# Optimization experiments

Measured on AMD Instinct MI355X. Metric: run time of the kernel, lower is better.

The kernel has to match this reference:

```python
import jax, jax.numpy as jnp
import numpy as np

NBINS = 128


def setup_inputs() -> dict:
    key = jax.random.key(0)
    feats = jax.random.normal(key, (100000, 8), dtype=jnp.float32)
    return {"feats": feats}


def reference(feats):
    # feats: [N, V]. setup=True path: fmin/fmax computed from feats itself.
    nvars = feats.shape[1]
    fmin = feats.min(axis=0)  # [V]
    fmax = feats.max(axis=0)  # [V]
    # torch.linspace(min, max, nbins) per variable -> [V, NBINS]
    t = jnp.arange(NBINS, dtype=feats.dtype) / (NBINS - 1)
    lin = fmin[:, None] + (fmax - fmin)[:, None] * t[None, :]
    step = lin[:, 1] - lin[:, 0]  # [V]
    # dense diff matrix, rounded to 6 decimals (np.around = round-half-even)
    diff = jnp.round((lin[None, :, :] - feats[:, :, None]) * 1e6) / 1e6  # [N, V, NBINS]
    # torch: cur_diff[cur_diff > 0] = cur_diff.min()  (min over that var's whole [N, NBINS] slab)
    mn = diff.min(axis=(0, 2), keepdims=True)  # [1, V, 1]
    masked = jnp.where(diff > 0, mn, diff)
    bins = jnp.argmax(masked, axis=2)  # [N, V], first max like torch
    # value of the chosen bin edge per sample/var
    vals = lin[jnp.arange(nvars)[None, :], bins]  # [N, V]
    regs = jnp.clip(feats - vals, 0.0, None) / step[None, :]
    return bins, regs
```

## Files before the change

kernel.cpp:

```cpp
#include <hip/hip_runtime.h>
#include <math.h>

#define NV 8
#define NBINS 128
#define GRID_A 64


__global__ __launch_bounds__(256) void k_colminmax(const float* __restrict__ feats,
                                                   float* __restrict__ ws, int n) {
    const int tid = threadIdx.x;
    const int gt = blockIdx.x * blockDim.x + tid;
    const int nth = blockDim.x * gridDim.x;
    float lmin[NV], lmax[NV];
#pragma unroll
    for (int c = 0; c < NV; ++c) { lmin[c] = __builtin_inff(); lmax[c] = -__builtin_inff(); }
    const int n4 = n >> 2;
    const float4* f4 = (const float4*)feats;
    if (((gt << 2) & 7) == 0) {
        for (int q = gt; q < n4; q += nth) {
            float4 v = f4[q];
            lmin[0] = fminf(lmin[0], v.x); lmax[0] = fmaxf(lmax[0], v.x);
            lmin[1] = fminf(lmin[1], v.y); lmax[1] = fmaxf(lmax[1], v.y);
            lmin[2] = fminf(lmin[2], v.z); lmax[2] = fmaxf(lmax[2], v.z);
            lmin[3] = fminf(lmin[3], v.w); lmax[3] = fmaxf(lmax[3], v.w);
        }
    } else {
        for (int q = gt; q < n4; q += nth) {
            float4 v = f4[q];
            lmin[4] = fminf(lmin[4], v.x); lmax[4] = fmaxf(lmax[4], v.x);
            lmin[5] = fminf(lmin[5], v.y); lmax[5] = fmaxf(lmax[5], v.y);
            lmin[6] = fminf(lmin[6], v.z); lmax[6] = fmaxf(lmax[6], v.z);
            lmin[7] = fminf(lmin[7], v.w); lmax[7] = fmaxf(lmax[7], v.w);
        }
    }
    for (int i = (n4 << 2) + gt; i < n; i += nth) {
        float v = feats[i];
        int c = i & 7;
#pragma unroll
        for (int cc = 0; cc < NV; ++cc)
            if (cc == c) { lmin[cc] = fminf(lmin[cc], v); lmax[cc] = fmaxf(lmax[cc], v); }
    }
#pragma unroll
    for (int c = 0; c < NV; ++c) {
        float mn = lmin[c], mx = lmax[c];
#pragma unroll
        for (int m = 32; m >= 1; m >>= 1) {
            mn = fminf(mn, __shfl_xor(mn, m));
            mx = fmaxf(mx, __shfl_xor(mx, m));
        }
        lmin[c] = mn; lmax[c] = mx;
    }
    __shared__ float smin[4][NV], smax[4][NV];
    const int wave = tid >> 6, lane = tid & 63;
    if (lane == 0) {
#pragma unroll
        for (int c = 0; c < NV; ++c) { smin[wave][c] = lmin[c]; smax[wave][c] = lmax[c]; }
    }
    __syncthreads();
    if (tid < NV) {
        float mn = fminf(fminf(smin[0][tid], smin[1][tid]), fminf(smin[2][tid], smin[3][tid]));
        float mx = fmaxf(fmaxf(smax[0][tid], smax[1][tid]), fmaxf(smax[2][tid], smax[3][tid]));
        ws[blockIdx.x * NV + tid] = mn;
        ws[GRID_A * NV + blockIdx.x * NV + tid] = mx;
    }
}

__global__ __launch_bounds__(64) void k_combine(float* __restrict__ ws) {
    const int t = threadIdx.x;
    float mn[NV], mx[NV];
#pragma unroll
    for (int c = 0; c < NV; ++c) {
        mn[c] = ws[t * NV + c];
        mx[c] = ws[GRID_A * NV + t * NV + c];
    }
#pragma unroll
    for (int c = 0; c < NV; ++c) {
#pragma unroll
        for (int m = 32; m >= 1; m >>= 1) {
            mn[c] = fminf(mn[c], __shfl_xor(mn[c], m));
            mx[c] = fmaxf(mx[c], __shfl_xor(mx[c], m));
        }
    }
    if (t == 0) {
#pragma unroll
        for (int c = 0; c < NV; ++c) {
            ws[2 * GRID_A * NV + c] = mn[c];
            ws[2 * GRID_A * NV + NV + c] = mx[c];
        }
    }
}

__global__ __launch_bounds__(256) void k_quantize(const float* __restrict__ feats,
                                                  const float* __restrict__ ws,
                                                  float* __restrict__ out, int n) {
    __shared__ float slin[NV * 129];
    __shared__ float sfmin[NV], sstep[NV];
    const int tid = threadIdx.x;
    const float* fm = ws + 2 * GRID_A * NV;
    for (int e = tid; e < NV * NBINS; e += blockDim.x) {
        int v = e >> 7;
        int b = e & 127;
        float fmin = fm[v];
        float range = __fsub_rn(fm[NV + v], fmin);
        float tb = __fdiv_rn((float)b, 127.0f);
        slin[v * 129 + b] = __fadd_rn(fmin, __fmul_rn(range, tb));
    }
    __syncthreads();
    if (tid < NV) {
        sfmin[tid] = slin[tid * 129 + 0];
        sstep[tid] = __fsub_rn(slin[tid * 129 + 1], slin[tid * 129 + 0]);
    }
    __syncthreads();
    const int i = blockIdx.x * blockDim.x + tid;
    if (i >= n) return;
    const int v = i & 7;
    const float feat = feats[i];
    const float fmin = sfmin[v];
    const float step = sstep[v];
    const float* lv = &slin[v * 129];
    int b = (int)floorf((feat - fmin) / step);
    b = b < 0 ? 0 : (b > 127 ? 127 : b);
    while (b < NBINS - 1 &&
           rintf(__fmul_rn(__fsub_rn(lv[b + 1], feat), 1.0e6f)) <= 0.0f) ++b;
    while (b > 0 &&
           rintf(__fmul_rn(__fsub_rn(lv[b], feat), 1.0e6f)) > 0.0f) --b;
    const float val = lv[b];
    const float reg = __fdiv_rn(fmaxf(__fsub_rn(feat, val), 0.0f), step);
    out[i] = (float)b;
    out[n + i] = reg;
}

extern "C" void kernel_launch(void* const* d_in, const int* in_sizes, int n_in,
                              void* d_out, int out_size, void* d_ws, size_t ws_size,
                              hipStream_t stream) {
    const float* feats = (const float*)d_in[0];
    float* ws = (float*)d_ws;
    float* out = (float*)d_out;
    const int n = in_sizes[0];
    k_colminmax<<<GRID_A, 256, 0, stream>>>(feats, ws, n);
    k_combine<<<1, 64, 0, stream>>>(ws);
    k_quantize<<<(n + 255) / 256, 256, 0, stream>>>(feats, ws, out, n);
}
```

Baseline: 69.89 us.

## Fuse min/max reduction and quantize into one persistent kernel with grid barrier

Replaces the three launches (column min/max, combine, quantize) with a single persistent kernel of 256 blocks of 512 threads. An atomic-counter grid barrier lets every block reduce the per-block partials itself and then quantize with a grid-stride loop. This removes two kernel launches and the dependency gaps between them. It relies on all 256 blocks being co-resident, and the spin barrier has a timeout that could silently produce wrong results if blocks are not all resident. It also replaces the per-element divide in the bin guess with a reciprocal multiply, which the correction loops then fix up.

```diff
diff --git a/kernel.cpp b/kernel.cpp
--- a/kernel.cpp
+++ b/kernel.cpp
@@ -3,21 +3,30 @@
 
 #define NV 8
 #define NBINS 128
-#define GRID_A 64
+#define GRID 256
+#define BLK 512
+#define NWAVE (BLK / 64)
 
+__device__ float g_pmin[GRID][NV];
+__device__ float g_pmax[GRID][NV];
+__device__ unsigned g_cnt = 0;
+__device__ unsigned g_gen = 0;
 
-__global__ __launch_bounds__(256) void k_colminmax(const float* __restrict__ feats,
-                                                   float* __restrict__ ws, int n) {
+__global__ __launch_bounds__(BLK) void k_fused(const float* __restrict__ feats,
+                                               float* __restrict__ out, int n) {
     const int tid = threadIdx.x;
-    const int gt = blockIdx.x * blockDim.x + tid;
-    const int nth = blockDim.x * gridDim.x;
+    const int bid = blockIdx.x;
+    const int gid = bid * BLK + tid;
+    const int nth = GRID * BLK;
+    const int wave = tid >> 6, lane = tid & 63;
+
     float lmin[NV], lmax[NV];
 #pragma unroll
     for (int c = 0; c < NV; ++c) { lmin[c] = __builtin_inff(); lmax[c] = -__builtin_inff(); }
     const int n4 = n >> 2;
     const float4* f4 = (const float4*)feats;
-    if (((gt << 2) & 7) == 0) {
-        for (int q = gt; q < n4; q += nth) {
+    if (((gid << 2) & 7) == 0) {
+        for (int q = gid; q < n4; q += nth) {
             float4 v = f4[q];
             lmin[0] = fminf(lmin[0], v.x); lmax[0] = fmaxf(lmax[0], v.x);
             lmin[1] = fminf(lmin[1], v.y); lmax[1] = fmaxf(lmax[1], v.y);
@@ -25,7 +34,7 @@
             lmin[3] = fminf(lmin[3], v.w); lmax[3] = fmaxf(lmax[3], v.w);
         }
     } else {
-        for (int q = gt; q < n4; q += nth) {
+        for (int q = gid; q < n4; q += nth) {
             float4 v = f4[q];
             lmin[4] = fminf(lmin[4], v.x); lmax[4] = fmaxf(lmax[4], v.x);
             lmin[5] = fminf(lmin[5], v.y); lmax[5] = fmaxf(lmax[5], v.y);
@@ -33,7 +42,7 @@
             lmin[7] = fminf(lmin[7], v.w); lmax[7] = fmaxf(lmax[7], v.w);
         }
     }
-    for (int i = (n4 << 2) + gt; i < n; i += nth) {
+    for (int i = (n4 << 2) + gid; i < n; i += nth) {
         float v = feats[i];
         int c = i & 7;
 #pragma unroll
@@ -50,94 +59,119 @@
         }
         lmin[c] = mn; lmax[c] = mx;
     }
-    __shared__ float smin[4][NV], smax[4][NV];
-    const int wave = tid >> 6, lane = tid & 63;
+    __shared__ float smin[NWAVE][NV], smax[NWAVE][NV];
     if (lane == 0) {
 #pragma unroll
         for (int c = 0; c < NV; ++c) { smin[wave][c] = lmin[c]; smax[wave][c] = lmax[c]; }
     }
     __syncthreads();
     if (tid < NV) {
-        float mn = fminf(fminf(smin[0][tid], smin[1][tid]), fminf(smin[2][tid], smin[3][tid]));
-        float mx = fmaxf(fmaxf(smax[0][tid], smax[1][tid]), fmaxf(smax[2][tid], smax[3][tid]));
-        ws[blockIdx.x * NV + tid] = mn;
-        ws[GRID_A * NV + blockIdx.x * NV + tid] = mx;
+        float mn = __builtin_inff(), mx = -__builtin_inff();
+#pragma unroll
+        for (int w = 0; w < NWAVE; ++w) {
+            mn = fminf(mn, smin[w][tid]);
+            mx = fmaxf(mx, smax[w][tid]);
+        }
+        __hip_atomic_store(&g_pmin[bid][tid], mn, __ATOMIC_RELAXED, __HIP_MEMORY_SCOPE_AGENT);
+        __hip_atomic_store(&g_pmax[bid][tid], mx, __ATOMIC_RELAXED, __HIP_MEMORY_SCOPE_AGENT);
     }
-}
+    __syncthreads();
 
-__global__ __launch_bounds__(64) void k_combine(float* __restrict__ ws) {
-    const int t = threadIdx.x;
-    float mn[NV], mx[NV];
-#pragma unroll
-    for (int c = 0; c < NV; ++c) {
-        mn[c] = ws[t * NV + c];
-        mx[c] = ws[GRID_A * NV + t * NV + c];
+    if (tid == 0) {
+        __threadfence();
+        unsigned my = __hip_atomic_load(&g_gen, __ATOMIC_RELAXED, __HIP_MEMORY_SCOPE_AGENT);
+        unsigned prev = __hip_atomic_fetch_add(&g_cnt, 1u, __ATOMIC_ACQ_REL, __HIP_MEMORY_SCOPE_AGENT);
+        if (prev == GRID - 1) {
+            __hip_atomic_store(&g_cnt, 0u, __ATOMIC_RELAXED, __HIP_MEMORY_SCOPE_AGENT);
+            __hip_atomic_fetch_add(&g_gen, 1u, __ATOMIC_RELEASE, __HIP_MEMORY_SCOPE_AGENT);
+        } else {
+            int spins = 0;
+            while (__hip_atomic_load(&g_gen, __ATOMIC_ACQUIRE, __HIP_MEMORY_SCOPE_AGENT) == my) {
+                __builtin_amdgcn_s_sleep(2);
+                if (++spins > (1 << 22)) break;
+            }
+        }
+        __threadfence();
     }
-#pragma unroll
-    for (int c = 0; c < NV; ++c) {
-#pragma unroll
-        for (int m = 32; m >= 1; m >>= 1) {
-            mn[c] = fminf(mn[c], __shfl_xor(mn[c], m));
-            mx[c] = fmaxf(mx[c], __shfl_xor(mx[c], m));
-        }
-    }
-    if (t == 0) {
+    __syncthreads();
+
+    __shared__ float cmin[4][NV], cmax[4][NV];
+    __shared__ float sgmin[NV], sgmax[NV];
+    if (wave < 4) {
+        const int pb = (wave << 6) | lane;
+        float mn[NV], mx[NV];
 #pragma unroll
         for (int c = 0; c < NV; ++c) {
-            ws[2 * GRID_A * NV + c] = mn[c];
-            ws[2 * GRID_A * NV + NV + c] = mx[c];
+            mn[c] = __hip_atomic_load(&g_pmin[pb][c], __ATOMIC_RELAXED, __HIP_MEMORY_SCOPE_AGENT);
+            mx[c] = __hip_atomic_load(&g_pmax[pb][c], __ATOMIC_RELAXED, __HIP_MEMORY_SCOPE_AGENT);
         }
-    }
-}
-
-__global__ __launch_bounds__(256) void k_quantize(const float* __restrict__ feats,
-                                                  const float* __restrict__ ws,
-                                                  float* __restrict__ out, int n) {
-    __shared__ float slin[NV * 129];
-    __shared__ float sfmin[NV], sstep[NV];
-    const int tid = threadIdx.x;
-    const float* fm = ws + 2 * GRID_A * NV;
-    for (int e = tid; e < NV * NBINS; e += blockDim.x) {
-        int v = e >> 7;
-        int b = e & 127;
-        float fmin = fm[v];
-        float range = __fsub_rn(fm[NV + v], fmin);
-        float tb = __fdiv_rn((float)b, 127.0f);
-        slin[v * 129 + b] = __fadd_rn(fmin, __fmul_rn(range, tb));
+#pragma unroll
+        for (int c = 0; c < NV; ++c) {
+#pragma unroll
+            for (int m = 32; m >= 1; m >>= 1) {
+                mn[c] = fminf(mn[c], __shfl_xor(mn[c], m));
+                mx[c] = fmaxf(mx[c], __shfl_xor(mx[c], m));
+            }
+        }
+        if (lane == 0) {
+#pragma unroll
+            for (int c = 0; c < NV; ++c) { cmin[wave][c] = mn[c]; cmax[wave][c] = mx[c]; }
+        }
     }
     __syncthreads();
     if (tid < NV) {
-        sfmin[tid] = slin[tid * 129 + 0];
-        sstep[tid] = __fsub_rn(slin[tid * 129 + 1], slin[tid * 129 + 0]);
+        sgmin[tid] = fminf(fminf(cmin[0][tid], cmin[1][tid]), fminf(cmin[2][tid], cmin[3][tid]));
+        sgmax[tid] = fmaxf(fmaxf(cmax[0][tid], cmax[1][tid]), fmaxf(cmax[2][tid], cmax[3][tid]));
     }
     __syncthreads();
-    const int i = blockIdx.x * blockDim.x + tid;
-    if (i >= n) return;
-    const int v = i & 7;
-    const float feat = feats[i];
-    const float fmin = sfmin[v];
+
+    __shared__ float slin[NV * 129];
+    __shared__ float sfmin[NV], sstep[NV], srstep[NV];
+    for (int e = tid; e < NV * NBINS; e += BLK) {
+        int v = e >> 7;
+        int b = e & 127;
+        float fmn = sgmin[v];
+        float range = __fsub_rn(sgmax[v], fmn);
+        float tb = __fdiv_rn((float)b, 127.0f);
+        slin[v * 129 + b] = __fadd_rn(fmn, __fmul_rn(range, tb));
+    }
+    __syncthreads();
+    if (tid < NV) {
+        float s0 = slin[tid * 129 + 0];
+        float s1 = slin[tid * 129 + 1];
+        sfmin[tid] = s0;
+        float st = __fsub_rn(s1, s0);
+        sstep[tid] = st;
+        srstep[tid] = __fdiv_rn(1.0f, st);
+    }
+    __syncthreads();
+
+    const int v = gid & 7;
+    const float fmn = sfmin[v];
     const float step = sstep[v];
+    const float rstep = srstep[v];
     const float* lv = &slin[v * 129];
-    int b = (int)floorf((feat - fmin) / step);
-    b = b < 0 ? 0 : (b > 127 ? 127 : b);
-    while (b < NBINS - 1 &&
-           rintf(__fmul_rn(__fsub_rn(lv[b + 1], feat), 1.0e6f)) <= 0.0f) ++b;
-    while (b > 0 &&
-           rintf(__fmul_rn(__fsub_rn(lv[b], feat), 1.0e6f)) > 0.0f) --b;
-    const float val = lv[b];
-    const float reg = __fdiv_rn(fmaxf(__fsub_rn(feat, val), 0.0f), step);
-    out[i] = (float)b;
-    out[n + i] = reg;
+    for (int i = gid; i < n; i += nth) {
+        const float feat = feats[i];
+        int b = (int)floorf(__fmul_rn(__fsub_rn(feat, fmn), rstep));
+        b = b < 0 ? 0 : (b > 127 ? 127 : b);
+        while (b < NBINS - 1 &&
+               rintf(__fmul_rn(__fsub_rn(lv[b + 1], feat), 1.0e6f)) <= 0.0f) ++b;
+        while (b > 0 &&
+               rintf(__fmul_rn(__fsub_rn(lv[b], feat), 1.0e6f)) > 0.0f) --b;
+        const float val = lv[b];
+        const float reg = __fdiv_rn(fmaxf(__fsub_rn(feat, val), 0.0f), step);
+        out[i] = (float)b;
+        out[n + i] = reg;
+    }
 }
 
 extern "C" void kernel_launch(void* const* d_in, const int* in_sizes, int n_in,
                               void* d_out, int out_size, void* d_ws, size_t ws_size,
                               hipStream_t stream) {
     const float* feats = (const float*)d_in[0];
-    float* ws = (float*)d_ws;
     float* out = (float*)d_out;
     const int n = in_sizes[0];
-    k_colminmax<<<GRID_A, 256, 0, stream>>>(feats, ws, n);
-    k_combine<<<1, 64, 0, stream>>>(ws);
-    k_quantize<<<(n + 255) / 256, 256, 0, stream>>>(feats, ws, out, n);
+    (void)d_ws; (void)ws_size;
+    k_fused<<<GRID, BLK, 0, stream>>>(feats, out, n);
 }
```

After: 89.22 us. 27.7% more time.

## Fuse min/max combine into quantize kernel with grid-stride loop

Applied to the files above, without the earlier changes.

Removes the single-block combine kernel by having each quantize block reduce the 64 partial min/max values itself from the workspace. The quantize kernel now uses a fixed grid of 1024 blocks with a grid-stride loop, which amortises the per-block linspace table setup over more elements. The initial bin guess multiplies by a precomputed reciprocal step instead of dividing. The trade-off is that every block repeats the small reduction, and the reciprocal guess is still corrected by the existing search loops.

```diff
diff --git a/kernel.cpp b/kernel.cpp
--- a/kernel.cpp
+++ b/kernel.cpp
@@ -4,6 +4,8 @@
 #define NV 8
 #define NBINS 128
 #define GRID_A 64
+#define GRID_Q 1024
+#define BLK_Q 256
 
 
 __global__ __launch_bounds__(256) void k_colminmax(const float* __restrict__ feats,
@@ -65,69 +67,76 @@
     }
 }
 
-__global__ __launch_bounds__(64) void k_combine(float* __restrict__ ws) {
-    const int t = threadIdx.x;
-    float mn[NV], mx[NV];
+__global__ __launch_bounds__(BLK_Q) void k_quantize2(const float* __restrict__ feats,
+                                                     const float* __restrict__ ws,
+                                                     float* __restrict__ out, int n) {
+    __shared__ float sgmin[NV], sgmax[NV];
+    __shared__ float slin[NV * 129];
+    __shared__ float sfmin[NV], sstep[NV], srstep[NV];
+    const int tid = threadIdx.x;
+
+    if (tid < 64) {
+        const float4* w4 = (const float4*)ws;
+        float4 a  = w4[2 * tid];
+        float4 b4 = w4[2 * tid + 1];
+        float4 c4 = w4[2 * GRID_A + 2 * tid];
+        float4 d4 = w4[2 * GRID_A + 2 * tid + 1];
+        float mn[NV] = {a.x, a.y, a.z, a.w, b4.x, b4.y, b4.z, b4.w};
+        float mx[NV] = {c4.x, c4.y, c4.z, c4.w, d4.x, d4.y, d4.z, d4.w};
 #pragma unroll
-    for (int c = 0; c < NV; ++c) {
-        mn[c] = ws[t * NV + c];
-        mx[c] = ws[GRID_A * NV + t * NV + c];
-    }
+        for (int c = 0; c < NV; ++c) {
 #pragma unroll
-    for (int c = 0; c < NV; ++c) {
+            for (int m = 32; m >= 1; m >>= 1) {
+                mn[c] = fminf(mn[c], __shfl_xor(mn[c], m));
+                mx[c] = fmaxf(mx[c], __shfl_xor(mx[c], m));
+            }
+        }
+        if (tid == 0) {
 #pragma unroll
-        for (int m = 32; m >= 1; m >>= 1) {
-            mn[c] = fminf(mn[c], __shfl_xor(mn[c], m));
-            mx[c] = fmaxf(mx[c], __shfl_xor(mx[c], m));
+            for (int c = 0; c < NV; ++c) { sgmin[c] = mn[c]; sgmax[c] = mx[c]; }
         }
     }
-    if (t == 0) {
-#pragma unroll
-        for (int c = 0; c < NV; ++c) {
-            ws[2 * GRID_A * NV + c] = mn[c];
-            ws[2 * GRID_A * NV + NV + c] = mx[c];
-        }
-    }
-}
+    __syncthreads();
 
-__global__ __launch_bounds__(256) void k_quantize(const float* __restrict__ feats,
-                                                  const float* __restrict__ ws,
-                                                  float* __restrict__ out, int n) {
-    __shared__ float slin[NV * 129];
-    __shared__ float sfmin[NV], sstep[NV];
-    const int tid = threadIdx.x;
-    const float* fm = ws + 2 * GRID_A * NV;
-    for (int e = tid; e < NV * NBINS; e += blockDim.x) {
+    for (int e = tid; e < NV * NBINS; e += BLK_Q) {
         int v = e >> 7;
         int b = e & 127;
-        float fmin = fm[v];
-        float range = __fsub_rn(fm[NV + v], fmin);
+        float fmn = sgmin[v];
+        float range = __fsub_rn(sgmax[v], fmn);
         float tb = __fdiv_rn((float)b, 127.0f);
-        slin[v * 129 + b] = __fadd_rn(fmin, __fmul_rn(range, tb));
+        slin[v * 129 + b] = __fadd_rn(fmn, __fmul_rn(range, tb));
     }
     __syncthreads();
     if (tid < NV) {
-        sfmin[tid] = slin[tid * 129 + 0];
-        sstep[tid] = __fsub_rn(slin[tid * 129 + 1], slin[tid * 129 + 0]);
+        float s0 = slin[tid * 129 + 0];
+        float s1 = slin[tid * 129 + 1];
+        sfmin[tid] = s0;
+        float st = __fsub_rn(s1, s0);
+        sstep[tid] = st;
+        srstep[tid] = __fdiv_rn(1.0f, st);
     }
     __syncthreads();
-    const int i = blockIdx.x * blockDim.x + tid;
-    if (i >= n) return;
-    const int v = i & 7;
-    const float feat = feats[i];
-    const float fmin = sfmin[v];
+
+    const int gid = blockIdx.x * BLK_Q + tid;
+    const int nth = GRID_Q * BLK_Q;
+    const int v = gid & 7;
+    const float fmn = sfmin[v];
     const float step = sstep[v];
+    const float rstep = srstep[v];
     const float* lv = &slin[v * 129];
-    int b = (int)floorf((feat - fmin) / step);
-    b = b < 0 ? 0 : (b > 127 ? 127 : b);
-    while (b < NBINS - 1 &&
-           rintf(__fmul_rn(__fsub_rn(lv[b + 1], feat), 1.0e6f)) <= 0.0f) ++b;
-    while (b > 0 &&
-           rintf(__fmul_rn(__fsub_rn(lv[b], feat), 1.0e6f)) > 0.0f) --b;
-    const float val = lv[b];
-    const float reg = __fdiv_rn(fmaxf(__fsub_rn(feat, val), 0.0f), step);
-    out[i] = (float)b;
-    out[n + i] = reg;
+    for (int i = gid; i < n; i += nth) {
+        const float feat = feats[i];
+        int b = (int)floorf(__fmul_rn(__fsub_rn(feat, fmn), rstep));
+        b = b < 0 ? 0 : (b > 127 ? 127 : b);
+        while (b < NBINS - 1 &&
+               rintf(__fmul_rn(__fsub_rn(lv[b + 1], feat), 1.0e6f)) <= 0.0f) ++b;
+        while (b > 0 &&
+               rintf(__fmul_rn(__fsub_rn(lv[b], feat), 1.0e6f)) > 0.0f) --b;
+        const float val = lv[b];
+        const float reg = __fdiv_rn(fmaxf(__fsub_rn(feat, val), 0.0f), step);
+        out[i] = (float)b;
+        out[n + i] = reg;
+    }
 }
 
 extern "C" void kernel_launch(void* const* d_in, const int* in_sizes, int n_in,
@@ -138,6 +147,5 @@
     float* out = (float*)d_out;
     const int n = in_sizes[0];
     k_colminmax<<<GRID_A, 256, 0, stream>>>(feats, ws, n);
-    k_combine<<<1, 64, 0, stream>>>(ws);
-    k_quantize<<<(n + 255) / 256, 256, 0, stream>>>(feats, ws, out, n);
+    k_quantize2<<<GRID_Q, BLK_Q, 0, stream>>>(feats, ws, out, n);
 }
```

Result: faster. 67.18 us (-3.9%).
